# Kernel optimization log

Measured on AMD Instinct MI355X. Metric: run time of the kernel, lower is better.

## Reference

```python
import jax, jax.numpy as jnp
import numpy as np

K = 5  # spline kernel size per dim (dim=3 -> 125 kernels)
N1, E1 = 10000, 60000
N2, E2 = 2500, 15000
N3, E3 = 625, 3750
N4, E4 = 160, 960
NC = 4  # num part classes (ShapeNet 'Pistol')


def spline_conv(x, ei, u, W, R, b):
    """SplineConv with degree-1 open B-splines, dim=3, kernel_size=K.
    x: [N, in], ei: [2, E] (src, dst), u: [E, 3] pseudo coords in [0,1],
    W: [K^3, in, out], R: [in, out] root weight, b: [out] bias.
    Mean-normalized neighborhood aggregation (norm=True) + root + bias."""
    src, dst = ei[0], ei[1]
    N, E = x.shape[0], ei.shape[1]
    v = u * (K - 1)
    k0f = jnp.clip(jnp.floor(v), 0.0, K - 2)
    f = v - k0f  # fractional offsets in [0, 1]
    k0 = k0f.astype(jnp.int32)
    # Pre-transform node features by every kernel: z[n, k, o]
    z = jnp.einsum('ni,kio->nko', x, W)
    msg = jnp.zeros((E, W.shape[2]), x.dtype)
    for b0 in (0, 1):
        for b1 in (0, 1):
            for b2 in (0, 1):
                idx = (k0[:, 0] + b0) * K * K + (k0[:, 1] + b1) * K + (k0[:, 2] + b2)
                wgt = ((f[:, 0] if b0 else 1.0 - f[:, 0]) *
                       (f[:, 1] if b1 else 1.0 - f[:, 1]) *
                       (f[:, 2] if b2 else 1.0 - f[:, 2]))
                msg = msg + wgt[:, None] * z[src, idx]
    agg = jax.ops.segment_sum(msg, dst, num_segments=N)
    deg = jax.ops.segment_sum(jnp.ones((E,), x.dtype), dst, num_segments=N)
    return agg / jnp.maximum(deg, 1.0)[:, None] + x @ R + b


def _net(x, u1, u2, u3, u4, w1, r1, b1, w12, r12, b12, w2, r2, b2, w22, r22, b22,
         w3, r3, b3, w32, r32, b32, w4, r4, b4, w42, r42, b42, w5, r5, b5,
         w6, r6, b6, w7, r7, b7, fc1w, fc1b, fc2w, fc2b,
         sk1w, sk1b, sk2w, sk2b, sk3w, sk3b, ei1, ei2, ei3, ei4, c1, c2, c3):
    elu = jax.nn.elu
    h1 = elu(spline_conv(x, ei1, u1, w1, r1, b1))
    h1 = elu(spline_conv(h1, ei1, u1, w12, r12, b12))
    h2 = jnp.concatenate([jax.ops.segment_max(h1, c1, num_segments=N2),
                          jnp.ones((N2, 1), x.dtype)], axis=1)
    h2 = elu(spline_conv(h2, ei2, u2, w2, r2, b2))
    h2 = elu(spline_conv(h2, ei2, u2, w22, r22, b22))
    h3 = jnp.concatenate([jax.ops.segment_max(h2, c2, num_segments=N3),
                          jnp.ones((N3, 1), x.dtype)], axis=1)
    h3 = elu(spline_conv(h3, ei3, u3, w3, r3, b3))
    h3 = elu(spline_conv(h3, ei3, u3, w32, r32, b32))
    h4 = jnp.concatenate([jax.ops.segment_max(h3, c3, num_segments=N4),
                          jnp.ones((N4, 1), x.dtype)], axis=1)
    h4 = elu(spline_conv(h4, ei4, u4, w4, r4, b4))
    h4 = elu(spline_conv(h4, ei4, u4, w42, r42, b42))
    h4 = elu(spline_conv(h4, ei4, u4, w42, r42, b42))  # conv42 applied twice, as in source
    h4 = elu(h4 @ fc1w + fc1b)  # dropout omitted (eval mode)
    g3 = elu(spline_conv(h4[c3] + h3 @ sk3w + sk3b, ei3, u3, w5, r5, b5))
    g2 = elu(spline_conv(g3[c2] + h2 @ sk2w + sk2b, ei2, u2, w6, r6, b6))
    g1 = elu(spline_conv(g2[c1] + h1 @ sk1w + sk1b, ei1, u1, w7, r7, b7))
    return jax.nn.log_softmax(g1 @ fc2w + fc2b, axis=1)


def setup_inputs() -> dict:
    key = jax.random.key(0)
    ks = iter(jax.random.split(key, 96))

    def nrm(shape, s=0.1):
        return jax.random.normal(next(ks), shape, jnp.float32) * s

    def edges(E, N):
        return jax.random.randint(next(ks), (2, E), 0, N, dtype=jnp.int32)

    def clus(Nl, Nn):
        # surjective cluster assignment so every pooled voxel is non-empty
        extra = jax.random.randint(next(ks), (Nl - Nn,), 0, Nn, dtype=jnp.int32)
        return jnp.concatenate([jnp.arange(Nn, dtype=jnp.int32), extra])

    d = {}
    d['x'] = nrm((N1, 1), 1.0)
    d['ei1'], d['u1'] = edges(E1, N1), jax.random.uniform(next(ks), (E1, 3), jnp.float32)
    d['ei2'], d['u2'] = edges(E2, N2), jax.random.uniform(next(ks), (E2, 3), jnp.float32)
    d['ei3'], d['u3'] = edges(E3, N3), jax.random.uniform(next(ks), (E3, 3), jnp.float32)
    d['ei4'], d['u4'] = edges(E4, N4), jax.random.uniform(next(ks), (E4, 3), jnp.float32)
    d['c1'], d['c2'], d['c3'] = clus(N1, N2), clus(N2, N3), clus(N3, N4)
    KK = K ** 3
    for name, cin, cout in [('1', 1, 64), ('12', 64, 64), ('2', 65, 64), ('22', 64, 64),
                            ('3', 65, 64), ('32', 64, 64), ('4', 65, 64), ('42', 64, 64),
                            ('5', 32, 32), ('6', 32, 32), ('7', 32, 32)]:
        d['w' + name] = nrm((KK, cin, cout))
        d['r' + name] = nrm((cin, cout))
        d['b' + name] = jnp.zeros((cout,), jnp.float32)
    d['fc1w'], d['fc1b'] = nrm((64, 32)), jnp.zeros((32,), jnp.float32)
    d['fc2w'], d['fc2b'] = nrm((32, NC)), jnp.zeros((NC,), jnp.float32)
    for s in ('1', '2', '3'):
        d['sk' + s + 'w'] = nrm((64, 32))
        d['sk' + s + 'b'] = jnp.zeros((32,), jnp.float32)
    return d


def reference(x, u1, u2, u3, u4, w1, r1, b1, w12, r12, b12, w2, r2, b2, w22, r22, b22,
              w3, r3, b3, w32, r32, b32, w4, r4, b4, w42, r42, b42, w5, r5, b5,
              w6, r6, b6, w7, r7, b7, fc1w, fc1b, fc2w, fc2b,
              sk1w, sk1b, sk2w, sk2b, sk3w, sk3b, ei1, ei2, ei3, ei4, c1, c2, c3):
    return _net(x, u1, u2, u3, u4, w1, r1, b1, w12, r12, b12, w2, r2, b2, w22, r22, b22,
                w3, r3, b3, w32, r32, b32, w4, r4, b4, w42, r42, b42, w5, r5, b5,
                w6, r6, b6, w7, r7, b7, fc1w, fc1b, fc2w, fc2b,
                sk1w, sk1b, sk2w, sk2b, sk3w, sk3b, ei1, ei2, ei3, ei4, c1, c2, c3)
```

## Files before the change

### kernel.cpp

```cpp
#include <hip/hip_runtime.h>
#include <math.h>


static const int N1 = 10000, E1 = 60000;
static const int N2 = 2500,  E2 = 15000;
static const int N3 = 625,   E3 = 3750;
static const int N4 = 160,   E4 = 960;
static const int NC = 4;
static const int CHUNK = 64;

typedef __attribute__((ext_vector_type(8))) short bfrag;
typedef __attribute__((ext_vector_type(4))) float f32x4;

__device__ __forceinline__ float eluf(float x) { return x > 0.f ? x : expm1f(x); }

__device__ __forceinline__ unsigned short bfc(float f) {
    unsigned u = __float_as_uint(f);
    return (unsigned short)((u + 0x7FFF + ((u >> 16) & 1)) >> 16);
}

struct InitArgs {
    const float* wsrc[10]; unsigned short* wdst[10];
    int cinmat[10], xs_[10], cout[10];
    long welems[10];
    long wtot;
    float* pools[3]; int pM[3];
    float* agg; int aggN4;
    int* preblk; int preN;
    int bB, bC, bD;
};

__global__ __launch_bounds__(256) void init_misc(InitArgs A) {
    const int blk = blockIdx.x, tid = threadIdx.x;
    if (blk < A.bB) {
        const long t = (long)blk * 256 + tid;
        if (t >= A.wtot) return;
        int k = 0;
        while (t >= A.welems[k]) ++k;
        const long base = k ? A.welems[k - 1] : 0;
        const long i2 = t - base;
        const int co = A.cout[k], cm = A.cinmat[k], xs = A.xs_[k];
        const int o = (int)(i2 % co);
        const long rest = i2 / co;
        const int i = (int)(rest % cm);
        const int kk = (int)(rest / cm);
        const float v = A.wsrc[k][((size_t)kk * xs + i) * co + o];
        const int KG = cm >> 3;
        A.wdst[k][(((size_t)(kk * KG + (i >> 3))) * co + o) * 8 + (i & 7)] = bfc(v);
    } else if (blk < A.bC) {
        const int t = (blk - A.bB) * 256 + tid;
        if (t >= A.pM[2]) return;
        const int p = (t < A.pM[0]) ? 0 : (t < A.pM[1] ? 1 : 2);
        const int base = p ? A.pM[p - 1] : 0;
        const int i2 = t - base;
        A.pools[p][i2] = (i2 % 65 == 64) ? 1.0f : -INFINITY;
    } else if (blk < A.bD) {
        const int t = (blk - A.bC) * 256 + tid;
        if (t < A.aggN4) ((float4*)A.agg)[t] = make_float4(0.f, 0.f, 0.f, 0.f);
    } else {
        const int t = (blk - A.bD) * 256 + tid;
        if (t < A.preN) A.preblk[t] = 0;
    }
}

struct Levels {
    const float* u[4]; const int* ei[4]; int E[4];
    int nb0[5];
    int cb0[5];
    int mc[4];
    int* ek0[4]; int* hist[4]; int* cursor[4]; float* deg[4];
    int* bchunk0[4]; int* ck0[4]; int* ccnt[4]; int* perm[4];
};

__global__ __launch_bounds__(256) void prep_conv1(Levels L, const float* __restrict__ x,
                                                  const float* __restrict__ w1,
                                                  float* __restrict__ agg, int nbTot) {
    __shared__ int lh[64];
    const int tid = threadIdx.x;
    if ((int)blockIdx.x < nbTot) {
        int l = 0;
        while (l < 3 && (int)blockIdx.x >= L.nb0[l + 1]) ++l;
        const int bl = blockIdx.x - L.nb0[l];
        if (tid < 64) lh[tid] = 0;
        __syncthreads();
        const int e = bl * 256 + tid;
        if (e < L.E[l]) {
            int b = 0;
            #pragma unroll
            for (int d = 0; d < 3; ++d) {
                const float v = L.u[l][e * 3 + d] * 4.0f;
                const float kf = fminf(fmaxf(floorf(v), 0.f), 3.f);
                b = (b << 2) | (int)kf;
            }
            L.ek0[l][e] = b;
            atomicAdd(&lh[b], 1);
            atomicAdd(&L.deg[l][L.ei[l][L.E[l] + e]], 1.0f);
        }
        __syncthreads();
        if (tid < 64 && lh[tid]) atomicAdd(&L.hist[l][tid], lh[tid]);
    } else {
        const int t = (blockIdx.x - nbTot) * 256 + tid;
        const int e = t >> 6, o = t & 63;
        if (e >= E1) return;
        const int src = L.ei[0][e], dst = L.ei[0][E1 + e];
        float f[3]; int kb = 0;
        #pragma unroll
        for (int d = 0; d < 3; ++d) {
            const float v = L.u[0][e * 3 + d] * 4.0f;
            const float kf = fminf(fmaxf(floorf(v), 0.f), 3.f);
            f[d] = v - kf; kb = kb * 5 + (int)kf;
        }
        float s = 0.f;
        #pragma unroll
        for (int c = 0; c < 8; ++c) {
            const int b0 = (c >> 2) & 1, b1 = (c >> 1) & 1, b2 = c & 1;
            const float wgt = (b0 ? f[0] : 1.f - f[0]) * (b1 ? f[1] : 1.f - f[1]) *
                              (b2 ? f[2] : 1.f - f[2]);
            s += wgt * w1[(size_t)(kb + b0 * 25 + b1 * 5 + b2) * 64 + o];
        }
        atomicAdd(&agg[(size_t)dst * 64 + o], x[src] * s);
    }
}

__global__ void scan_all(Levels L) {
    const int l = blockIdx.x;
    __shared__ int sb[65];
    const int t = threadIdx.x;
    if (t == 0) {
        int cc = 0;
        for (int b = 0; b < 64; ++b) { sb[b] = cc; cc += (L.hist[l][b] + CHUNK - 1) / CHUNK; }
        sb[64] = cc;
    }
    __syncthreads();
    L.bchunk0[l][t] = sb[t];
    if (t == 0) L.bchunk0[l][64] = sb[64];
}

__global__ __launch_bounds__(256) void fill_scatter_node1(
        Levels L, const float* __restrict__ x, float* __restrict__ agg,
        const float* __restrict__ r1, const float* __restrict__ b1,
        float* __restrict__ h1a, int cbTot, int nbTot) {
    __shared__ int lh[64], lbase[64];
    const int tid = threadIdx.x;
    const int blk = blockIdx.x;
    if (blk < cbTot) {
        int l = 0;
        while (l < 3 && blk >= L.cb0[l + 1]) ++l;
        const int c = (blk - L.cb0[l]) * 256 + tid;
        if (c >= L.mc[l]) return;
        const int* bchunk0 = L.bchunk0[l];
        if (c >= bchunk0[64]) { L.ccnt[l][c] = 0; L.ck0[l][c] = 0; return; }
        int lo = 0, hi = 64;
        while (hi - lo > 1) { int m = (lo + hi) >> 1; if (bchunk0[m] <= c) lo = m; else hi = m; }
        const int j = c - bchunk0[lo];
        L.ck0[l][c] = lo;
        L.ccnt[l][c] = min(CHUNK, L.hist[l][lo] - j * CHUNK);
    } else if (blk < cbTot + nbTot) {
        const int fb = blk - cbTot;
        int l = 0;
        while (l < 3 && fb >= L.nb0[l + 1]) ++l;
        const int bl = fb - L.nb0[l];
        if (tid < 64) lh[tid] = 0;
        __syncthreads();
        const int e = bl * 256 + tid;
        int b = -1, r = 0;
        if (e < L.E[l]) { b = L.ek0[l][e]; r = atomicAdd(&lh[b], 1); }
        __syncthreads();
        if (tid < 64) lbase[tid] = lh[tid] ? atomicAdd(&L.cursor[l][tid], lh[tid]) : 0;
        __syncthreads();
        if (e < L.E[l]) L.perm[l][L.bchunk0[l][b] * CHUNK + lbase[b] + r] = e;
    } else {
        const int nb = blk - cbTot - nbTot;
        const int lane = tid & 63;
        const int grp  = tid >> 6;
        const int n = nb * 4 + grp;
        if (n >= N1) return;
        const float d = fmaxf(L.deg[0][n], 1.f);
        const size_t idx = (size_t)n * 64 + lane;
        float s = agg[idx] / d + b1[lane];
        agg[idx] = 0.f;
        s += x[n] * r1[lane];
        h1a[idx] = eluf(s);
    }
}

template<int CINMAT, int COUT, bool HAS_ONES>
__global__ __launch_bounds__(256) void bucket_gemm(
        const float* __restrict__ x, const int* __restrict__ ei, const float* __restrict__ u,
        const unsigned short* __restrict__ Wt, const float* __restrict__ Wf,
        const int* __restrict__ perm, const int* __restrict__ ck0, const int* __restrict__ ccnt,
        float* __restrict__ agg, int E) {
    constexpr int ALDA = CINMAT + 8;
    constexpr int KG   = CINMAT / 8;
    constexpr int NT   = COUT / 16;
    constexpr int HALVES = CINMAT / 32;
    constexpr int XS   = CINMAT + (HAS_ONES ? 1 : 0);
    constexpr int IT   = CINMAT / 4;

    __shared__ unsigned short A0s[64 * ALDA], A1s[64 * ALDA];
    __shared__ float gS[64 * 4], sS[64 * 2];
    __shared__ int srcS[64], dstS[64];
    __shared__ float WonesS[HAS_ONES ? 8 * COUT : 4];

    const int chunk = blockIdx.x;
    const int cnt = ccnt[chunk];
    if (cnt == 0) return;
    const int b = ck0[chunk];
    const int kbase = ((b >> 4) & 3) * 25 + ((b >> 2) & 3) * 5 + (b & 3);
    const int cstart = chunk * CHUNK;
    const int tid = threadIdx.x;

    if (tid < CHUNK) {
        const int e = tid;
        const int pe = (e < cnt) ? perm[cstart + e] : -1;
        int sv = -1, dv = 0;
        float g0 = 0, g1 = 0, g2 = 0, g3 = 0, s0 = 0, s1 = 0;
        if (pe >= 0) {
            sv = ei[pe]; dv = ei[E + pe];
            float f[3];
            #pragma unroll
            for (int d2 = 0; d2 < 3; ++d2) {
                const float v = u[pe * 3 + d2] * 4.f;
                const float kf = fminf(fmaxf(floorf(v), 0.f), 3.f);
                f[d2] = v - kf;
            }
            g0 = (1.f - f[0]) * (1.f - f[1]); g1 = (1.f - f[0]) * f[1];
            g2 = f[0] * (1.f - f[1]);         g3 = f[0] * f[1];
            s0 = 1.f - f[2]; s1 = f[2];
        }
        srcS[e] = sv; dstS[e] = dv;
        gS[e * 4 + 0] = g0; gS[e * 4 + 1] = g1; gS[e * 4 + 2] = g2; gS[e * 4 + 3] = g3;
        sS[e * 2 + 0] = s0; sS[e * 2 + 1] = s1;
    }
    if (HAS_ONES) {
        for (int t2 = tid; t2 < 8 * COUT; t2 += 256) {
            const int c = t2 / COUT, o = t2 % COUT;
            const int koff = ((c >> 2) & 1) * 25 + ((c >> 1) & 1) * 5 + (c & 1);
            WonesS[t2] = Wf[((size_t)(kbase + koff) * XS + CINMAT) * COUT + o];
        }
    }
    __syncthreads();

    {
        const int e  = tid >> 2;
        const int ib = (tid & 3) * IT;
        const int sv = srcS[e];
        const float sc0 = sS[e * 2], sc1 = sS[e * 2 + 1];
        #pragma unroll
        for (int j = 0; j < IT; j += 2) {
            float x0 = 0.f, x1 = 0.f;
            if (sv >= 0) {
                x0 = x[(size_t)sv * XS + ib + j];
                x1 = x[(size_t)sv * XS + ib + j + 1];
            }
            const unsigned p0 = bfc(x0 * sc0) | ((unsigned)bfc(x1 * sc0) << 16);
            const unsigned p1 = bfc(x0 * sc1) | ((unsigned)bfc(x1 * sc1) << 16);
            *(unsigned*)&A0s[e * ALDA + ib + j] = p0;
            *(unsigned*)&A1s[e * ALDA + ib + j] = p1;
        }
    }
    __syncthreads();

    const int lane = tid & 63;
    const int wid  = tid >> 6;
    const int m0   = wid * 16;
    const int arow = m0 + (lane & 15);
    const int kg   = lane >> 4;
    const int ocol = lane & 15;

    f32x4 acc[4][NT];
    #pragma unroll
    for (int q = 0; q < 4; ++q)
        #pragma unroll
        for (int nt = 0; nt < NT; ++nt) acc[q][nt] = (f32x4){0.f, 0.f, 0.f, 0.f};

    #pragma unroll
    for (int q = 0; q < 4; ++q) {
        #pragma unroll
        for (int b2 = 0; b2 < 2; ++b2) {
            const unsigned short* Ab = b2 ? A1s : A0s;
            const int koff = (q >> 1) * 25 + (q & 1) * 5 + b2;
            #pragma unroll
            for (int hf = 0; hf < HALVES; ++hf) {
                const bfrag a = *(const bfrag*)(Ab + arow * ALDA + hf * 32 + kg * 8);
                const int krow = (kbase + koff) * KG + hf * 4 + kg;
                #pragma unroll
                for (int nt = 0; nt < NT; ++nt) {
                    const bfrag bb = *(const bfrag*)(Wt + ((size_t)krow * COUT + nt * 16 + ocol) * 8);
                    acc[q][nt] = __builtin_amdgcn_mfma_f32_16x16x32_bf16(a, bb, acc[q][nt], 0, 0, 0);
                }
            }
        }
    }

    const int grp = lane >> 4;
    #pragma unroll
    for (int nt = 0; nt < NT; ++nt) {
        const int o = nt * 16 + ocol;
        float wo[8];
        if (HAS_ONES) {
            #pragma unroll
            for (int c = 0; c < 8; ++c) wo[c] = WonesS[c * COUT + o];
        }
        #pragma unroll
        for (int r = 0; r < 4; ++r) {
            const int e = m0 + grp * 4 + r;
            if (e < cnt) {
                const float g0 = gS[e * 4 + 0], g1 = gS[e * 4 + 1];
                const float g2 = gS[e * 4 + 2], g3 = gS[e * 4 + 3];
                float v = g0 * acc[0][nt][r] + g1 * acc[1][nt][r] +
                          g2 * acc[2][nt][r] + g3 * acc[3][nt][r];
                if (HAS_ONES) {
                    const float s0v = sS[e * 2], s1v = sS[e * 2 + 1];
                    v += g0 * (s0v * wo[0] + s1v * wo[1]) + g1 * (s0v * wo[2] + s1v * wo[3]) +
                         g2 * (s0v * wo[4] + s1v * wo[5]) + g3 * (s0v * wo[6] + s1v * wo[7]);
                }
                atomicAdd(&agg[(size_t)dstS[e] * COUT + o], v);
            }
        }
    }
}

enum { NODE_PLAIN = 0, NODE_SEGMAX = 1, NODE_FC1 = 2, NODE_LSM = 3 };

template<int CIN, int COUT, int MODE>
__global__ void spline_node_f(const float* __restrict__ x, float* __restrict__ agg,
                              const float* __restrict__ deg, const float* __restrict__ R,
                              const float* __restrict__ b, float* __restrict__ out, int N,
                              const int* __restrict__ cl, float* __restrict__ pool,
                              const float* __restrict__ fw, const float* __restrict__ fb2,
                              float* __restrict__ fout) {
    constexpr int NPB = 256 / COUT;
    __shared__ float rowbuf[NPB][COUT];
    const int lane = threadIdx.x % COUT;
    const int grp  = threadIdx.x / COUT;
    const int n = blockIdx.x * NPB + grp;
    if (n >= N) return;
    const float d = fmaxf(deg[n], 1.f);
    const size_t idx = (size_t)n * COUT + lane;
    float s = agg[idx] / d + b[lane];
    agg[idx] = 0.f;
    const float* xs = x + (size_t)n * CIN;
    #pragma unroll 4
    for (int i = 0; i < CIN; ++i) s += xs[i] * R[i * COUT + lane];
    const float val = eluf(s);
    if (MODE == NODE_PLAIN || MODE == NODE_SEGMAX) out[idx] = val;
    if (MODE == NODE_SEGMAX) {
        float* addr = pool + (size_t)cl[n] * 65 + lane;
        if (val >= 0.f) atomicMax((int*)addr, __float_as_int(val));
        else            atomicMin((unsigned int*)addr, __float_as_uint(val));
    }
    if (MODE == NODE_FC1) {
        rowbuf[grp][lane] = val;
        if (lane < 32) {
            float s2 = fb2[lane];
            #pragma unroll 4
            for (int i = 0; i < 64; ++i) s2 += rowbuf[grp][i] * fw[i * 32 + lane];
            fout[(size_t)n * 32 + lane] = eluf(s2);
        }
    }
    if (MODE == NODE_LSM) {
        float p[NC];
        #pragma unroll
        for (int o = 0; o < NC; ++o) p[o] = val * fw[lane * NC + o];
        #pragma unroll
        for (int m = 16; m >= 1; m >>= 1)
            #pragma unroll
            for (int o = 0; o < NC; ++o) p[o] += __shfl_xor(p[o], m, 32);
        #pragma unroll
        for (int o = 0; o < NC; ++o) p[o] += fb2[o];
        const float mx = fmaxf(fmaxf(p[0], p[1]), fmaxf(p[2], p[3]));
        float se = 0.f;
        #pragma unroll
        for (int o = 0; o < NC; ++o) se += expf(p[o] - mx);
        const float lg = logf(se);
        if (lane < NC) fout[(size_t)n * NC + lane] = p[lane] - mx - lg;
    }
}

__global__ void skip_gather(const float* __restrict__ up, const int* __restrict__ cl,
                            const float* __restrict__ h, const float* __restrict__ skw,
                            const float* __restrict__ skb, float* __restrict__ out, int N) {
    const int lane = threadIdx.x & 31;
    const int grp  = threadIdx.x >> 5;
    const int n = blockIdx.x * 8 + grp;
    if (n >= N) return;
    float s = up[(size_t)cl[n] * 32 + lane] + skb[lane];
    const float* hs = h + (size_t)n * 64;
    #pragma unroll 4
    for (int i = 0; i < 64; ++i) s += hs[i] * skw[i * 32 + lane];
    out[(size_t)n * 32 + lane] = s;
}

struct HLevel {
    const int* ei; const float* u; int E; int maxchunks;
    int *ek0, *hist, *cursor, *bchunk0, *ck0, *ccnt, *perm;
    float* deg;
};

extern "C" void kernel_launch(void* const* d_in, const int* in_sizes, int n_in,
                              void* d_out, int out_size, void* d_ws, size_t ws_size,
                              hipStream_t stream) {
    const float* x    = (const float*)d_in[0];
    const int*   ei1  = (const int*)  d_in[1];
    const float* u1   = (const float*)d_in[2];
    const int*   ei2  = (const int*)  d_in[3];
    const float* u2   = (const float*)d_in[4];
    const int*   ei3  = (const int*)  d_in[5];
    const float* u3   = (const float*)d_in[6];
    const int*   ei4  = (const int*)  d_in[7];
    const float* u4   = (const float*)d_in[8];
    const int*   c1   = (const int*)  d_in[9];
    const int*   c2   = (const int*)  d_in[10];
    const int*   c3   = (const int*)  d_in[11];
    const float *w1  = (const float*)d_in[12], *r1  = (const float*)d_in[13], *b1  = (const float*)d_in[14];
    const float *w12 = (const float*)d_in[15], *r12 = (const float*)d_in[16], *b12 = (const float*)d_in[17];
    const float *w2  = (const float*)d_in[18], *r2  = (const float*)d_in[19], *b2  = (const float*)d_in[20];
    const float *w22 = (const float*)d_in[21], *r22 = (const float*)d_in[22], *b22 = (const float*)d_in[23];
    const float *w3  = (const float*)d_in[24], *r3  = (const float*)d_in[25], *b3  = (const float*)d_in[26];
    const float *w32 = (const float*)d_in[27], *r32 = (const float*)d_in[28], *b32 = (const float*)d_in[29];
    const float *w4  = (const float*)d_in[30], *r4  = (const float*)d_in[31], *b4  = (const float*)d_in[32];
    const float *w42 = (const float*)d_in[33], *r42 = (const float*)d_in[34], *b42 = (const float*)d_in[35];
    const float *w5  = (const float*)d_in[36], *r5  = (const float*)d_in[37], *b5  = (const float*)d_in[38];
    const float *w6  = (const float*)d_in[39], *r6  = (const float*)d_in[40], *b6  = (const float*)d_in[41];
    const float *w7  = (const float*)d_in[42], *r7  = (const float*)d_in[43], *b7  = (const float*)d_in[44];
    const float *fc1w = (const float*)d_in[45], *fc1b = (const float*)d_in[46];
    const float *fc2w = (const float*)d_in[47], *fc2b = (const float*)d_in[48];
    const float *sk1w = (const float*)d_in[49], *sk1b = (const float*)d_in[50];
    const float *sk2w = (const float*)d_in[51], *sk2b = (const float*)d_in[52];
    const float *sk3w = (const float*)d_in[53], *sk3b = (const float*)d_in[54];
    float* out = (float*)d_out;

    char* wsb = (char*)d_ws;
    size_t off = 0;
    auto alloc = [&](size_t bytes) {
        void* p = wsb + off; off = (off + bytes + 255) & ~(size_t)255; return p;
    };
    auto allocF = [&](size_t n) { return (float*)alloc(n * 4); };
    auto allocI = [&](size_t n) { return (int*)alloc(n * 4); };
    auto allocH = [&](size_t n) { return (unsigned short*)alloc(n * 2); };

    float* h1a  = allocF((size_t)N1 * 64);
    float* h1   = allocF((size_t)N1 * 64);
    float* h2in = allocF((size_t)N2 * 65);
    float* h2a  = allocF((size_t)N2 * 64);
    float* h2   = allocF((size_t)N2 * 64);
    float* h3in = allocF((size_t)N3 * 65);
    float* h3a  = allocF((size_t)N3 * 64);
    float* h3   = allocF((size_t)N3 * 64);
    float* h4in = allocF((size_t)N4 * 65);
    float* h4a  = allocF((size_t)N4 * 64);
    float* h4b  = allocF((size_t)N4 * 64);
    float* h4   = allocF((size_t)N4 * 32);
    float* g3in = allocF((size_t)N3 * 32);
    float* g3   = allocF((size_t)N3 * 32);
    float* g2in = allocF((size_t)N2 * 32);
    float* g2   = allocF((size_t)N2 * 32);
    float* g1in = allocF((size_t)N1 * 32);
    float* agg  = allocF((size_t)N1 * 64);

    const size_t SZ64 = (size_t)125 * 8 * 64 * 8;
    const size_t SZ32 = (size_t)125 * 4 * 32 * 8;
    unsigned short* t12 = allocH(SZ64);
    unsigned short* t22 = allocH(SZ64);
    unsigned short* t32 = allocH(SZ64);
    unsigned short* t42 = allocH(SZ64);
    unsigned short* t2  = allocH(SZ64);
    unsigned short* t3  = allocH(SZ64);
    unsigned short* t4  = allocH(SZ64);
    unsigned short* t5  = allocH(SZ32);
    unsigned short* t6  = allocH(SZ32);
    unsigned short* t7  = allocH(SZ32);

    HLevel L[4];
    const int*   eis[4] = {ei1, ei2, ei3, ei4};
    const float* us [4] = {u1, u2, u3, u4};
    const int    Es [4] = {E1, E2, E3, E4};
    const int    Ns [4] = {N1, N2, N3, N4};

    int preN = 0;
    for (int l = 0; l < 4; ++l) preN += 128 + Ns[l];
    int* preblk = allocI(preN);
    {
        int c = 0;
        for (int l = 0; l < 4; ++l) {
            L[l].ei = eis[l]; L[l].u = us[l]; L[l].E = Es[l];
            L[l].maxchunks = (Es[l] + CHUNK - 1) / CHUNK + 64;
            L[l].hist = preblk + c; L[l].cursor = preblk + c + 64;
            L[l].deg = (float*)(preblk + c + 128);
            c += 128 + Ns[l];
            L[l].ek0     = allocI(Es[l]);
            L[l].bchunk0 = allocI(65);
            L[l].ck0     = allocI(L[l].maxchunks);
            L[l].ccnt    = allocI(L[l].maxchunks);
            L[l].perm    = allocI((size_t)L[l].maxchunks * CHUNK);
        }
    }

    InitArgs IA;
    {
        const float* srcs[10] = {w12, w22, w32, w42, w2, w3, w4, w5, w6, w7};
        unsigned short* dsts[10] = {t12, t22, t32, t42, t2, t3, t4, t5, t6, t7};
        const int cms[10] = {64,64,64,64,64,64,64,32,32,32};
        const int xss[10] = {64,64,64,64,65,65,65,32,32,32};
        const int cos[10] = {64,64,64,64,64,64,64,32,32,32};
        long cum = 0;
        for (int k = 0; k < 10; ++k) {
            IA.wsrc[k] = srcs[k]; IA.wdst[k] = dsts[k];
            IA.cinmat[k] = cms[k]; IA.xs_[k] = xss[k]; IA.cout[k] = cos[k];
            cum += (long)125 * cms[k] * cos[k];
            IA.welems[k] = cum;
        }
        IA.wtot = cum;
        IA.pools[0] = h2in; IA.pools[1] = h3in; IA.pools[2] = h4in;
        IA.pM[0] = N2 * 65; IA.pM[1] = N2 * 65 + N3 * 65; IA.pM[2] = N2 * 65 + N3 * 65 + N4 * 65;
        IA.agg = agg; IA.aggN4 = N1 * 64 / 4;
        IA.preblk = preblk; IA.preN = preN;
        const int bA = (int)((IA.wtot + 255) / 256);
        const int bB = (IA.pM[2] + 255) / 256;
        const int bC = (IA.aggN4 + 255) / 256;
        const int bD = (preN + 255) / 256;
        IA.bB = bA; IA.bC = bA + bB; IA.bD = bA + bB + bC;
        init_misc<<<bA + bB + bC + bD, 256, 0, stream>>>(IA);
    }

    Levels DL;
    int nbTot = 0, cbTot = 0;
    {
        for (int l = 0; l < 4; ++l) {
            DL.u[l] = L[l].u; DL.ei[l] = L[l].ei; DL.E[l] = L[l].E;
            DL.nb0[l] = nbTot; nbTot += (L[l].E + 255) / 256;
            DL.cb0[l] = cbTot; cbTot += (L[l].maxchunks + 255) / 256;
            DL.mc[l] = L[l].maxchunks;
            DL.ek0[l] = L[l].ek0; DL.hist[l] = L[l].hist; DL.cursor[l] = L[l].cursor;
            DL.deg[l] = L[l].deg; DL.bchunk0[l] = L[l].bchunk0;
            DL.ck0[l] = L[l].ck0; DL.ccnt[l] = L[l].ccnt; DL.perm[l] = L[l].perm;
        }
        DL.nb0[4] = nbTot; DL.cb0[4] = cbTot;
        const int conv1B = (E1 * 64) / 256;
        prep_conv1<<<nbTot + conv1B, 256, 0, stream>>>(DL, x, w1, agg, nbTot);
        scan_all<<<4, 64, 0, stream>>>(DL);
        const int n1B = (N1 + 3) / 4;
        fill_scatter_node1<<<cbTot + nbTot + n1B, 256, 0, stream>>>(
            DL, x, agg, r1, b1, h1a, cbTot, nbTot);
    }

    bucket_gemm<64, 64, false><<<L[0].maxchunks, 256, 0, stream>>>(
        h1a, L[0].ei, L[0].u, t12, nullptr, L[0].perm, L[0].ck0, L[0].ccnt, agg, L[0].E);
    spline_node_f<64, 64, NODE_SEGMAX><<<(N1 + 3) / 4, 256, 0, stream>>>(
        h1a, agg, L[0].deg, r12, b12, h1, N1, c1, h2in, nullptr, nullptr, nullptr);

    bucket_gemm<64, 64, true><<<L[1].maxchunks, 256, 0, stream>>>(
        h2in, L[1].ei, L[1].u, t2, w2, L[1].perm, L[1].ck0, L[1].ccnt, agg, L[1].E);
    spline_node_f<65, 64, NODE_PLAIN><<<(N2 + 3) / 4, 256, 0, stream>>>(
        h2in, agg, L[1].deg, r2, b2, h2a, N2, nullptr, nullptr, nullptr, nullptr, nullptr);
    bucket_gemm<64, 64, false><<<L[1].maxchunks, 256, 0, stream>>>(
        h2a, L[1].ei, L[1].u, t22, nullptr, L[1].perm, L[1].ck0, L[1].ccnt, agg, L[1].E);
    spline_node_f<64, 64, NODE_SEGMAX><<<(N2 + 3) / 4, 256, 0, stream>>>(
        h2a, agg, L[1].deg, r22, b22, h2, N2, c2, h3in, nullptr, nullptr, nullptr);

    bucket_gemm<64, 64, true><<<L[2].maxchunks, 256, 0, stream>>>(
        h3in, L[2].ei, L[2].u, t3, w3, L[2].perm, L[2].ck0, L[2].ccnt, agg, L[2].E);
    spline_node_f<65, 64, NODE_PLAIN><<<(N3 + 3) / 4, 256, 0, stream>>>(
        h3in, agg, L[2].deg, r3, b3, h3a, N3, nullptr, nullptr, nullptr, nullptr, nullptr);
    bucket_gemm<64, 64, false><<<L[2].maxchunks, 256, 0, stream>>>(
        h3a, L[2].ei, L[2].u, t32, nullptr, L[2].perm, L[2].ck0, L[2].ccnt, agg, L[2].E);
    spline_node_f<64, 64, NODE_SEGMAX><<<(N3 + 3) / 4, 256, 0, stream>>>(
        h3a, agg, L[2].deg, r32, b32, h3, N3, c3, h4in, nullptr, nullptr, nullptr);

    bucket_gemm<64, 64, true><<<L[3].maxchunks, 256, 0, stream>>>(
        h4in, L[3].ei, L[3].u, t4, w4, L[3].perm, L[3].ck0, L[3].ccnt, agg, L[3].E);
    spline_node_f<65, 64, NODE_PLAIN><<<(N4 + 3) / 4, 256, 0, stream>>>(
        h4in, agg, L[3].deg, r4, b4, h4a, N4, nullptr, nullptr, nullptr, nullptr, nullptr);
    bucket_gemm<64, 64, false><<<L[3].maxchunks, 256, 0, stream>>>(
        h4a, L[3].ei, L[3].u, t42, nullptr, L[3].perm, L[3].ck0, L[3].ccnt, agg, L[3].E);
    spline_node_f<64, 64, NODE_PLAIN><<<(N4 + 3) / 4, 256, 0, stream>>>(
        h4a, agg, L[3].deg, r42, b42, h4b, N4, nullptr, nullptr, nullptr, nullptr, nullptr);
    bucket_gemm<64, 64, false><<<L[3].maxchunks, 256, 0, stream>>>(
        h4b, L[3].ei, L[3].u, t42, nullptr, L[3].perm, L[3].ck0, L[3].ccnt, agg, L[3].E);
    spline_node_f<64, 64, NODE_FC1><<<(N4 + 3) / 4, 256, 0, stream>>>(
        h4b, agg, L[3].deg, r42, b42, nullptr, N4, nullptr, nullptr, fc1w, fc1b, h4);

    skip_gather<<<(N3 + 7) / 8, 256, 0, stream>>>(h4, c3, h3, sk3w, sk3b, g3in, N3);
    bucket_gemm<32, 32, false><<<L[2].maxchunks, 256, 0, stream>>>(
        g3in, L[2].ei, L[2].u, t5, nullptr, L[2].perm, L[2].ck0, L[2].ccnt, agg, L[2].E);
    spline_node_f<32, 32, NODE_PLAIN><<<(N3 + 7) / 8, 256, 0, stream>>>(
        g3in, agg, L[2].deg, r5, b5, g3, N3, nullptr, nullptr, nullptr, nullptr, nullptr);

    skip_gather<<<(N2 + 7) / 8, 256, 0, stream>>>(g3, c2, h2, sk2w, sk2b, g2in, N2);
    bucket_gemm<32, 32, false><<<L[1].maxchunks, 256, 0, stream>>>(
        g2in, L[1].ei, L[1].u, t6, nullptr, L[1].perm, L[1].ck0, L[1].ccnt, agg, L[1].E);
    spline_node_f<32, 32, NODE_PLAIN><<<(N2 + 7) / 8, 256, 0, stream>>>(
        g2in, agg, L[1].deg, r6, b6, g2, N2, nullptr, nullptr, nullptr, nullptr, nullptr);

    skip_gather<<<(N1 + 7) / 8, 256, 0, stream>>>(g2, c1, h1, sk1w, sk1b, g1in, N1);
    bucket_gemm<32, 32, false><<<L[0].maxchunks, 256, 0, stream>>>(
        g1in, L[0].ei, L[0].u, t7, nullptr, L[0].perm, L[0].ck0, L[0].ccnt, agg, L[0].E);
    spline_node_f<32, 32, NODE_LSM><<<(N1 + 7) / 8, 256, 0, stream>>>(
        g1in, agg, L[0].deg, r7, b7, nullptr, N1, nullptr, nullptr, fc2w, fc2b, out);
}
```

Baseline: 284.1 us.

## Fuse skip-gather into consumers, fold scan into fill, vectorize weight conversion

Removes the skip_gather kernels by recomputing the skip linear layer (upsampled coarse features plus h times skw) inside both bucket_gemm's A-tile load and spline_node_f's root term. Removes the separate scan kernel by having each fill/scatter block recompute the chunk prefix sum in shared memory. Weight bf16 conversion now writes 8-element packed fragments per thread, and x loads in bucket_gemm use float4 when aligned. Eliminating launches and intermediate buffers trades for redundant per-edge recomputation of a 64x32 matvec in the level-1 skip layer, which may cost more than it saves.

Result: slower. 294.9 us (+3.8%).

```diff
diff --git a/kernel.cpp b/kernel.cpp
--- a/kernel.cpp
+++ b/kernel.cpp
@@ -37,16 +37,18 @@
         if (t >= A.wtot) return;
         int k = 0;
         while (t >= A.welems[k]) ++k;
-        const long base = k ? A.welems[k - 1] : 0;
-        const long i2 = t - base;
+        const long i2 = t - (k ? A.welems[k - 1] : 0);
         const int co = A.cout[k], cm = A.cinmat[k], xs = A.xs_[k];
+        const int KG = cm >> 3;
         const int o = (int)(i2 % co);
         const long rest = i2 / co;
-        const int i = (int)(rest % cm);
-        const int kk = (int)(rest / cm);
-        const float v = A.wsrc[k][((size_t)kk * xs + i) * co + o];
-        const int KG = cm >> 3;
-        A.wdst[k][(((size_t)(kk * KG + (i >> 3))) * co + o) * 8 + (i & 7)] = bfc(v);
+        const int g8 = (int)(rest % KG);
+        const int kk = (int)(rest / KG);
+        const float* sp = A.wsrc[k] + ((size_t)kk * xs + g8 * 8) * co + o;
+        bfrag bv;
+        #pragma unroll
+        for (int j = 0; j < 8; ++j) bv[j] = (short)bfc(sp[(size_t)j * co]);
+        *(bfrag*)(A.wdst[k] + (((size_t)(kk * KG + g8)) * co + o) * 8) = bv;
     } else if (blk < A.bC) {
         const int t = (blk - A.bB) * 256 + tid;
         if (t >= A.pM[2]) return;
@@ -69,7 +71,7 @@
     int cb0[5];
     int mc[4];
     int* ek0[4]; int* hist[4]; int* cursor[4]; float* deg[4];
-    int* bchunk0[4]; int* ck0[4]; int* ccnt[4]; int* perm[4];
+    int* ck0[4]; int* ccnt[4]; int* perm[4];
 };
 
 __global__ __launch_bounds__(256) void prep_conv1(Levels L, const float* __restrict__ x,
@@ -122,44 +124,43 @@
     }
 }
 
-__global__ void scan_all(Levels L) {
-    const int l = blockIdx.x;
-    __shared__ int sb[65];
-    const int t = threadIdx.x;
-    if (t == 0) {
-        int cc = 0;
-        for (int b = 0; b < 64; ++b) { sb[b] = cc; cc += (L.hist[l][b] + CHUNK - 1) / CHUNK; }
-        sb[64] = cc;
-    }
-    __syncthreads();
-    L.bchunk0[l][t] = sb[t];
-    if (t == 0) L.bchunk0[l][64] = sb[64];
-}
-
 __global__ __launch_bounds__(256) void fill_scatter_node1(
         Levels L, const float* __restrict__ x, float* __restrict__ agg,
         const float* __restrict__ r1, const float* __restrict__ b1,
         float* __restrict__ h1a, int cbTot, int nbTot) {
+    __shared__ int sb[65];
     __shared__ int lh[64], lbase[64];
     const int tid = threadIdx.x;
     const int blk = blockIdx.x;
     if (blk < cbTot) {
         int l = 0;
         while (l < 3 && blk >= L.cb0[l + 1]) ++l;
+        if (tid == 0) {
+            int cc = 0;
+            for (int b = 0; b < 64; ++b) { sb[b] = cc; cc += (L.hist[l][b] + CHUNK - 1) / CHUNK; }
+            sb[64] = cc;
+        }
+        __syncthreads();
         const int c = (blk - L.cb0[l]) * 256 + tid;
-        if (c >= L.mc[l]) return;
-        const int* bchunk0 = L.bchunk0[l];
-        if (c >= bchunk0[64]) { L.ccnt[l][c] = 0; L.ck0[l][c] = 0; return; }
-        int lo = 0, hi = 64;
-        while (hi - lo > 1) { int m = (lo + hi) >> 1; if (bchunk0[m] <= c) lo = m; else hi = m; }
-        const int j = c - bchunk0[lo];
-        L.ck0[l][c] = lo;
-        L.ccnt[l][c] = min(CHUNK, L.hist[l][lo] - j * CHUNK);
+        if (c < L.mc[l]) {
+            if (c >= sb[64]) { L.ccnt[l][c] = 0; L.ck0[l][c] = 0; }
+            else {
+                int lo = 0, hi = 64;
+                while (hi - lo > 1) { int m = (lo + hi) >> 1; if (sb[m] <= c) lo = m; else hi = m; }
+                const int j = c - sb[lo];
+                L.ck0[l][c] = lo;
+                L.ccnt[l][c] = min(CHUNK, L.hist[l][lo] - j * CHUNK);
+            }
+        }
     } else if (blk < cbTot + nbTot) {
         const int fb = blk - cbTot;
         int l = 0;
         while (l < 3 && fb >= L.nb0[l + 1]) ++l;
         const int bl = fb - L.nb0[l];
+        if (tid == 0) {
+            int cc = 0;
+            for (int b = 0; b < 64; ++b) { sb[b] = cc; cc += (L.hist[l][b] + CHUNK - 1) / CHUNK; }
+        }
         if (tid < 64) lh[tid] = 0;
         __syncthreads();
         const int e = bl * 256 + tid;
@@ -168,7 +169,7 @@
         __syncthreads();
         if (tid < 64) lbase[tid] = lh[tid] ? atomicAdd(&L.cursor[l][tid], lh[tid]) : 0;
         __syncthreads();
-        if (e < L.E[l]) L.perm[l][L.bchunk0[l][b] * CHUNK + lbase[b] + r] = e;
+        if (e < L.E[l]) L.perm[l][sb[b] * CHUNK + lbase[b] + r] = e;
     } else {
         const int nb = blk - cbTot - nbTot;
         const int lane = tid & 63;
@@ -184,12 +185,15 @@
     }
 }
 
-template<int CINMAT, int COUT, bool HAS_ONES>
+template<int CINMAT, int COUT, bool HAS_ONES, bool SKIP>
 __global__ __launch_bounds__(256) void bucket_gemm(
         const float* __restrict__ x, const int* __restrict__ ei, const float* __restrict__ u,
         const unsigned short* __restrict__ Wt, const float* __restrict__ Wf,
         const int* __restrict__ perm, const int* __restrict__ ck0, const int* __restrict__ ccnt,
-        float* __restrict__ agg, int E) {
+        float* __restrict__ agg, int E,
+        const float* __restrict__ up, const int* __restrict__ cl,
+        const float* __restrict__ hh, const float* __restrict__ skw,
+        const float* __restrict__ skb) {
     constexpr int ALDA = CINMAT + 8;
     constexpr int KG   = CINMAT / 8;
     constexpr int NT   = COUT / 16;
@@ -246,15 +250,36 @@
         const int ib = (tid & 3) * IT;
         const int sv = srcS[e];
         const float sc0 = sS[e * 2], sc1 = sS[e * 2 + 1];
+        float xv[IT];
+        if (SKIP) {
+            if (sv >= 0) {
+                #pragma unroll
+                for (int j = 0; j < IT; ++j) xv[j] = up[(size_t)cl[sv] * 32 + ib + j] + skb[ib + j];
+                #pragma unroll 4
+                for (int i = 0; i < 64; ++i) {
+                    const float hv = hh[(size_t)sv * 64 + i];
+                    #pragma unroll
+                    for (int j = 0; j < IT; ++j) xv[j] += hv * skw[i * 32 + ib + j];
+                }
+            } else {
+                #pragma unroll
+                for (int j = 0; j < IT; ++j) xv[j] = 0.f;
+            }
+        } else if ((XS & 3) == 0) {
+            #pragma unroll
+            for (int j = 0; j < IT; j += 4) {
+                float4 q = make_float4(0.f, 0.f, 0.f, 0.f);
+                if (sv >= 0) q = *(const float4*)&x[(size_t)sv * XS + ib + j];
+                xv[j] = q.x; xv[j + 1] = q.y; xv[j + 2] = q.z; xv[j + 3] = q.w;
+            }
+        } else {
+            #pragma unroll
+            for (int j = 0; j < IT; ++j) xv[j] = (sv >= 0) ? x[(size_t)sv * XS + ib + j] : 0.f;
+        }
         #pragma unroll
         for (int j = 0; j < IT; j += 2) {
-            float x0 = 0.f, x1 = 0.f;
-            if (sv >= 0) {
-                x0 = x[(size_t)sv * XS + ib + j];
-                x1 = x[(size_t)sv * XS + ib + j + 1];
-            }
-            const unsigned p0 = bfc(x0 * sc0) | ((unsigned)bfc(x1 * sc0) << 16);
-            const unsigned p1 = bfc(x0 * sc1) | ((unsigned)bfc(x1 * sc1) << 16);
+            const unsigned p0 = bfc(xv[j] * sc0) | ((unsigned)bfc(xv[j + 1] * sc0) << 16);
+            const unsigned p1 = bfc(xv[j] * sc1) | ((unsigned)bfc(xv[j + 1] * sc1) << 16);
             *(unsigned*)&A0s[e * ALDA + ib + j] = p0;
             *(unsigned*)&A1s[e * ALDA + ib + j] = p1;
         }
@@ -323,13 +348,16 @@
 
 enum { NODE_PLAIN = 0, NODE_SEGMAX = 1, NODE_FC1 = 2, NODE_LSM = 3 };
 
-template<int CIN, int COUT, int MODE>
+template<int CIN, int COUT, int MODE, bool SKIPIN>
 __global__ void spline_node_f(const float* __restrict__ x, float* __restrict__ agg,
                               const float* __restrict__ deg, const float* __restrict__ R,
                               const float* __restrict__ b, float* __restrict__ out, int N,
                               const int* __restrict__ cl, float* __restrict__ pool,
                               const float* __restrict__ fw, const float* __restrict__ fb2,
-                              float* __restrict__ fout) {
+                              float* __restrict__ fout,
+                              const int* __restrict__ skcl, const float* __restrict__ skup,
+                              const float* __restrict__ skh, const float* __restrict__ skww,
+                              const float* __restrict__ skbb) {
     constexpr int NPB = 256 / COUT;
     __shared__ float rowbuf[NPB][COUT];
     const int lane = threadIdx.x % COUT;
@@ -340,9 +368,19 @@
     const size_t idx = (size_t)n * COUT + lane;
     float s = agg[idx] / d + b[lane];
     agg[idx] = 0.f;
-    const float* xs = x + (size_t)n * CIN;
-    #pragma unroll 4
-    for (int i = 0; i < CIN; ++i) s += xs[i] * R[i * COUT + lane];
+    if (SKIPIN) {
+        float vi = skup[(size_t)skcl[n] * 32 + lane] + skbb[lane];
+        #pragma unroll 4
+        for (int i = 0; i < 64; ++i) vi += skh[(size_t)n * 64 + i] * skww[i * 32 + lane];
+        const int half = threadIdx.x & 32;
+        #pragma unroll
+        for (int i = 0; i < 32; ++i)
+            s += __shfl(vi, half + i, 64) * R[i * 32 + lane];
+    } else {
+        const float* xs = x + (size_t)n * CIN;
+        #pragma unroll 4
+        for (int i = 0; i < CIN; ++i) s += xs[i] * R[i * COUT + lane];
+    }
     const float val = eluf(s);
     if (MODE == NODE_PLAIN || MODE == NODE_SEGMAX) out[idx] = val;
     if (MODE == NODE_SEGMAX) {
@@ -378,23 +416,9 @@
     }
 }
 
-__global__ void skip_gather(const float* __restrict__ up, const int* __restrict__ cl,
-                            const float* __restrict__ h, const float* __restrict__ skw,
-                            const float* __restrict__ skb, float* __restrict__ out, int N) {
-    const int lane = threadIdx.x & 31;
-    const int grp  = threadIdx.x >> 5;
-    const int n = blockIdx.x * 8 + grp;
-    if (n >= N) return;
-    float s = up[(size_t)cl[n] * 32 + lane] + skb[lane];
-    const float* hs = h + (size_t)n * 64;
-    #pragma unroll 4
-    for (int i = 0; i < 64; ++i) s += hs[i] * skw[i * 32 + lane];
-    out[(size_t)n * 32 + lane] = s;
-}
-
 struct HLevel {
     const int* ei; const float* u; int E; int maxchunks;
-    int *ek0, *hist, *cursor, *bchunk0, *ck0, *ccnt, *perm;
+    int *ek0, *hist, *cursor, *ck0, *ccnt, *perm;
     float* deg;
 };
 
@@ -452,11 +476,8 @@
     float* h4a  = allocF((size_t)N4 * 64);
     float* h4b  = allocF((size_t)N4 * 64);
     float* h4   = allocF((size_t)N4 * 32);
-    float* g3in = allocF((size_t)N3 * 32);
     float* g3   = allocF((size_t)N3 * 32);
-    float* g2in = allocF((size_t)N2 * 32);
     float* g2   = allocF((size_t)N2 * 32);
-    float* g1in = allocF((size_t)N1 * 32);
     float* agg  = allocF((size_t)N1 * 64);
 
     const size_t SZ64 = (size_t)125 * 8 * 64 * 8;
@@ -490,7 +511,6 @@
             L[l].deg = (float*)(preblk + c + 128);
             c += 128 + Ns[l];
             L[l].ek0     = allocI(Es[l]);
-            L[l].bchunk0 = allocI(65);
             L[l].ck0     = allocI(L[l].maxchunks);
             L[l].ccnt    = allocI(L[l].maxchunks);
             L[l].perm    = allocI((size_t)L[l].maxchunks * CHUNK);
@@ -508,7 +528,7 @@
         for (int k = 0; k < 10; ++k) {
             IA.wsrc[k] = srcs[k]; IA.wdst[k] = dsts[k];
             IA.cinmat[k] = cms[k]; IA.xs_[k] = xss[k]; IA.cout[k] = cos[k];
-            cum += (long)125 * cms[k] * cos[k];
+            cum += (long)125 * (cms[k] / 8) * cos[k];
             IA.welems[k] = cum;
         }
         IA.wtot = cum;
@@ -533,69 +553,87 @@
             DL.cb0[l] = cbTot; cbTot += (L[l].maxchunks + 255) / 256;
             DL.mc[l] = L[l].maxchunks;
             DL.ek0[l] = L[l].ek0; DL.hist[l] = L[l].hist; DL.cursor[l] = L[l].cursor;
-            DL.deg[l] = L[l].deg; DL.bchunk0[l] = L[l].bchunk0;
+            DL.deg[l] = L[l].deg;
             DL.ck0[l] = L[l].ck0; DL.ccnt[l] = L[l].ccnt; DL.perm[l] = L[l].perm;
         }
         DL.nb0[4] = nbTot; DL.cb0[4] = cbTot;
         const int conv1B = (E1 * 64) / 256;
         prep_conv1<<<nbTot + conv1B, 256, 0, stream>>>(DL, x, w1, agg, nbTot);
-        scan_all<<<4, 64, 0, stream>>>(DL);
         const int n1B = (N1 + 3) / 4;
         fill_scatter_node1<<<cbTot + nbTot + n1B, 256, 0, stream>>>(
             DL, x, agg, r1, b1, h1a, cbTot, nbTot);
     }
 
-    bucket_gemm<64, 64, false><<<L[0].maxchunks, 256, 0, stream>>>(
-        h1a, L[0].ei, L[0].u, t12, nullptr, L[0].perm, L[0].ck0, L[0].ccnt, agg, L[0].E);
-    spline_node_f<64, 64, NODE_SEGMAX><<<(N1 + 3) / 4, 256, 0, stream>>>(
-        h1a, agg, L[0].deg, r12, b12, h1, N1, c1, h2in, nullptr, nullptr, nullptr);
-
-    bucket_gemm<64, 64, true><<<L[1].maxchunks, 256, 0, stream>>>(
-        h2in, L[1].ei, L[1].u, t2, w2, L[1].perm, L[1].ck0, L[1].ccnt, agg, L[1].E);
-    spline_node_f<65, 64, NODE_PLAIN><<<(N2 + 3) / 4, 256, 0, stream>>>(
-        h2in, agg, L[1].deg, r2, b2, h2a, N2, nullptr, nullptr, nullptr, nullptr, nullptr);
-    bucket_gemm<64, 64, false><<<L[1].maxchunks, 256, 0, stream>>>(
-        h2a, L[1].ei, L[1].u, t22, nullptr, L[1].perm, L[1].ck0, L[1].ccnt, agg, L[1].E);
-    spline_node_f<64, 64, NODE_SEGMAX><<<(N2 + 3) / 4, 256, 0, stream>>>(
-        h2a, agg, L[1].deg, r22, b22, h2, N2, c2, h3in, nullptr, nullptr, nullptr);
-
-    bucket_gemm<64, 64, true><<<L[2].maxchunks, 256, 0, stream>>>(
-        h3in, L[2].ei, L[2].u, t3, w3, L[2].perm, L[2].ck0, L[2].ccnt, agg, L[2].E);
-    spline_node_f<65, 64, NODE_PLAIN><<<(N3 + 3) / 4, 256, 0, stream>>>(
-        h3in, agg, L[2].deg, r3, b3, h3a, N3, nullptr, nullptr, nullptr, nullptr, nullptr);
-    bucket_gemm<64, 64, false><<<L[2].maxchunks, 256, 0, stream>>>(
-        h3a, L[2].ei, L[2].u, t32, nullptr, L[2].perm, L[2].ck0, L[2].ccnt, agg, L[2].E);
-    spline_node_f<64, 64, NODE_SEGMAX><<<(N3 + 3) / 4, 256, 0, stream>>>(
-        h3a, agg, L[2].deg, r32, b32, h3, N3, c3, h4in, nullptr, nullptr, nullptr);
-
-    bucket_gemm<64, 64, true><<<L[3].maxchunks, 256, 0, stream>>>(
-        h4in, L[3].ei, L[3].u, t4, w4, L[3].perm, L[3].ck0, L[3].ccnt, agg, L[3].E);
-    spline_node_f<65, 64, NODE_PLAIN><<<(N4 + 3) / 4, 256, 0, stream>>>(
-        h4in, agg, L[3].deg, r4, b4, h4a, N4, nullptr, nullptr, nullptr, nullptr, nullptr);
-    bucket_gemm<64, 64, false><<<L[3].maxchunks, 256, 0, stream>>>(
-        h4a, L[3].ei, L[3].u, t42, nullptr, L[3].perm, L[3].ck0, L[3].ccnt, agg, L[3].E);
-    spline_node_f<64, 64, NODE_PLAIN><<<(N4 + 3) / 4, 256, 0, stream>>>(
-        h4a, agg, L[3].deg, r42, b42, h4b, N4, nullptr, nullptr, nullptr, nullptr, nullptr);
-    bucket_gemm<64, 64, false><<<L[3].maxchunks, 256, 0, stream>>>(
-        h4b, L[3].ei, L[3].u, t42, nullptr, L[3].perm, L[3].ck0, L[3].ccnt, agg, L[3].E);
-    spline_node_f<64, 64, NODE_FC1><<<(N4 + 3) / 4, 256, 0, stream>>>(
-        h4b, agg, L[3].deg, r42, b42, nullptr, N4, nullptr, nullptr, fc1w, fc1b, h4);
-
-    skip_gather<<<(N3 + 7) / 8, 256, 0, stream>>>(h4, c3, h3, sk3w, sk3b, g3in, N3);
-    bucket_gemm<32, 32, false><<<L[2].maxchunks, 256, 0, stream>>>(
-        g3in, L[2].ei, L[2].u, t5, nullptr, L[2].perm, L[2].ck0, L[2].ccnt, agg, L[2].E);
-    spline_node_f<32, 32, NODE_PLAIN><<<(N3 + 7) / 8, 256, 0, stream>>>(
-        g3in, agg, L[2].deg, r5, b5, g3, N3, nullptr, nullptr, nullptr, nullptr, nullptr);
-
-    skip_gather<<<(N2 + 7) / 8, 256, 0, stream>>>(g3, c2, h2, sk2w, sk2b, g2in, N2);
-    bucket_gemm<32, 32, false><<<L[1].maxchunks, 256, 0, stream>>>(
-        g2in, L[1].ei, L[1].u, t6, nullptr, L[1].perm, L[1].ck0, L[1].ccnt, agg, L[1].E);
-    spline_node_f<32, 32, NODE_PLAIN><<<(N2 + 7) / 8, 256, 0, stream>>>(
-        g2in, agg, L[1].deg, r6, b6, g2, N2, nullptr, nullptr, nullptr, nullptr, nullptr);
-
-    skip_gather<<<(N1 + 7) / 8, 256, 0, stream>>>(g2, c1, h1, sk1w, sk1b, g1in, N1);
-    bucket_gemm<32, 32, false><<<L[0].maxchunks, 256, 0, stream>>>(
-        g1in, L[0].ei, L[0].u, t7, nullptr, L[0].perm, L[0].ck0, L[0].ccnt, agg, L[0].E);
-    spline_node_f<32, 32, NODE_LSM><<<(N1 + 7) / 8, 256, 0, stream>>>(
-        g1in, agg, L[0].deg, r7, b7, nullptr, N1, nullptr, nullptr, fc2w, fc2b, out);
+    bucket_gemm<64, 64, false, false><<<L[0].maxchunks, 256, 0, stream>>>(
+        h1a, L[0].ei, L[0].u, t12, nullptr, L[0].perm, L[0].ck0, L[0].ccnt, agg, L[0].E,
+        nullptr, nullptr, nullptr, nullptr, nullptr);
+    spline_node_f<64, 64, NODE_SEGMAX, false><<<(N1 + 3) / 4, 256, 0, stream>>>(
+        h1a, agg, L[0].deg, r12, b12, h1, N1, c1, h2in, nullptr, nullptr, nullptr,
+        nullptr, nullptr, nullptr, nullptr, nullptr);
+
+    bucket_gemm<64, 64, true, false><<<L[1].maxchunks, 256, 0, stream>>>(
+        h2in, L[1].ei, L[1].u, t2, w2, L[1].perm, L[1].ck0, L[1].ccnt, agg, L[1].E,
+        nullptr, nullptr, nullptr, nullptr, nullptr);
+    spline_node_f<65, 64, NODE_PLAIN, false><<<(N2 + 3) / 4, 256, 0, stream>>>(
+        h2in, agg, L[1].deg, r2, b2, h2a, N2, nullptr, nullptr, nullptr, nullptr, nullptr,
+        nullptr, nullptr, nullptr, nullptr, nullptr);
+    bucket_gemm<64, 64, false, false><<<L[1].maxchunks, 256, 0, stream>>>(
+        h2a, L[1].ei, L[1].u, t22, nullptr, L[1].perm, L[1].ck0, L[1].ccnt, agg, L[1].E,
+        nullptr, nullptr, nullptr, nullptr, nullptr);
+    spline_node_f<64, 64, NODE_SEGMAX, false><<<(N2 + 3) / 4, 256, 0, stream>>>(
+        h2a, agg, L[1].deg, r22, b22, h2, N2, c2, h3in, nullptr, nullptr, nullptr,
+        nullptr, nullptr, nullptr, nullptr, nullptr);
+
+    bucket_gemm<64, 64, true, false><<<L[2].maxchunks, 256, 0, stream>>>(
+        h3in, L[2].ei, L[2].u, t3, w3, L[2].perm, L[2].ck0, L[2].ccnt, agg, L[2].E,
+        nullptr, nullptr, nullptr, nullptr, nullptr);
+    spline_node_f<65, 64, NODE_PLAIN, false><<<(N3 + 3) / 4, 256, 0, stream>>>(
+        h3in, agg, L[2].deg, r3, b3, h3a, N3, nullptr, nullptr, nullptr, nullptr, nullptr,
+        nullptr, nullptr, nullptr, nullptr, nullptr);
+    bucket_gemm<64, 64, false, false><<<L[2].maxchunks, 256, 0, stream>>>(
+        h3a, L[2].ei, L[2].u, t32, nullptr, L[2].perm, L[2].ck0, L[2].ccnt, agg, L[2].E,
+        nullptr, nullptr, nullptr, nullptr, nullptr);
+    spline_node_f<64, 64, NODE_SEGMAX, false><<<(N3 + 3) / 4, 256, 0, stream>>>(
+        h3a, agg, L[2].deg, r32, b32, h3, N3, c3, h4in, nullptr, nullptr, nullptr,
+        nullptr, nullptr, nullptr, nullptr, nullptr);
+
+    bucket_gemm<64, 64, true, false><<<L[3].maxchunks, 256, 0, stream>>>(
+        h4in, L[3].ei, L[3].u, t4, w4, L[3].perm, L[3].ck0, L[3].ccnt, agg, L[3].E,
+        nullptr, nullptr, nullptr, nullptr, nullptr);
+    spline_node_f<65, 64, NODE_PLAIN, false><<<(N4 + 3) / 4, 256, 0, stream>>>(
+        h4in, agg, L[3].deg, r4, b4, h4a, N4, nullptr, nullptr, nullptr, nullptr, nullptr,
+        nullptr, nullptr, nullptr, nullptr, nullptr);
+    bucket_gemm<64, 64, false, false><<<L[3].maxchunks, 256, 0, stream>>>(
+        h4a, L[3].ei, L[3].u, t42, nullptr, L[3].perm, L[3].ck0, L[3].ccnt, agg, L[3].E,
+        nullptr, nullptr, nullptr, nullptr, nullptr);
+    spline_node_f<64, 64, NODE_PLAIN, false><<<(N4 + 3) / 4, 256, 0, stream>>>(
+        h4a, agg, L[3].deg, r42, b42, h4b, N4, nullptr, nullptr, nullptr, nullptr, nullptr,
+        nullptr, nullptr, nullptr, nullptr, nullptr);
+    bucket_gemm<64, 64, false, false><<<L[3].maxchunks, 256, 0, stream>>>(
+        h4b, L[3].ei, L[3].u, t42, nullptr, L[3].perm, L[3].ck0, L[3].ccnt, agg, L[3].E,
+        nullptr, nullptr, nullptr, nullptr, nullptr);
+    spline_node_f<64, 64, NODE_FC1, false><<<(N4 + 3) / 4, 256, 0, stream>>>(
+        h4b, agg, L[3].deg, r42, b42, nullptr, N4, nullptr, nullptr, fc1w, fc1b, h4,
+        nullptr, nullptr, nullptr, nullptr, nullptr);
+
+    bucket_gemm<32, 32, false, true><<<L[2].maxchunks, 256, 0, stream>>>(
+        nullptr, L[2].ei, L[2].u, t5, nullptr, L[2].perm, L[2].ck0, L[2].ccnt, agg, L[2].E,
+        h4, c3, h3, sk3w, sk3b);
+    spline_node_f<32, 32, NODE_PLAIN, true><<<(N3 + 7) / 8, 256, 0, stream>>>(
+        nullptr, agg, L[2].deg, r5, b5, g3, N3, nullptr, nullptr, nullptr, nullptr, nullptr,
+        c3, h4, h3, sk3w, sk3b);
+
+    bucket_gemm<32, 32, false, true><<<L[1].maxchunks, 256, 0, stream>>>(
+        nullptr, L[1].ei, L[1].u, t6, nullptr, L[1].perm, L[1].ck0, L[1].ccnt, agg, L[1].E,
+        g3, c2, h2, sk2w, sk2b);
+    spline_node_f<32, 32, NODE_PLAIN, true><<<(N2 + 7) / 8, 256, 0, stream>>>(
+        nullptr, agg, L[1].deg, r6, b6, g2, N2, nullptr, nullptr, nullptr, nullptr, nullptr,
+        c2, g3, h2, sk2w, sk2b);
+
+    bucket_gemm<32, 32, false, true><<<L[0].maxchunks, 256, 0, stream>>>(
+        nullptr, L[0].ei, L[0].u, t7, nullptr, L[0].perm, L[0].ck0, L[0].ccnt, agg, L[0].E,
+        g2, c1, h1, sk1w, sk1b);
+    spline_node_f<32, 32, NODE_LSM, true><<<(N1 + 7) / 8, 256, 0, stream>>>(
+        nullptr, agg, L[0].deg, r7, b7, nullptr, N1, nullptr, nullptr, fc2w, fc2b, out,
+        c1, g2, h1, sk1w, sk1b);
 }
```
